# Optimization experiments

Measured on AMD Instinct MI355X. Metric: run time of the kernel, lower is better.

The kernel has to match this reference:

```python
import jax, jax.numpy as jnp
import numpy as np

BINS = jnp.array([1, 2, 3, 4, 8, 16, 32, 64], dtype=jnp.int32)
L = 10      # max span width
HID = 150   # Score hidden dim


def _mlp(x, W1, b1, W2, b2, W3, b3):
    # Score module: Linear -> ReLU -> Linear -> ReLU -> Linear (dropout = identity at eval)
    h = jax.nn.relu(x @ W1 + b1)
    h = jax.nn.relu(h @ W2 + b2)
    return h @ W3 + b3


def setup_inputs() -> dict:
    key = jax.random.key(0)
    ks = jax.random.split(key, 16)
    T, A, E, D, S = 8192, 1024, 512, 20, 32768
    GI = 2 * A + E + D  # 2580
    sc = lambda n: 1.0 / np.sqrt(n)
    return {
        "states": jax.random.normal(ks[0], (T, A), jnp.float32),
        "embeds": jax.random.normal(ks[1], (T, E), jnp.float32),
        "span_starts": jnp.sort(jax.random.randint(ks[2], (S,), 0, T - L)),
        "span_lengths": jax.random.randint(ks[3], (S,), 0, L),
        # attention Score params (attn_dim -> 150 -> 150 -> 1)
        "Wa1": jax.random.normal(ks[4], (A, HID), jnp.float32) * sc(A),
        "ba1": jnp.zeros((HID,), jnp.float32),
        "Wa2": jax.random.normal(ks[5], (HID, HID), jnp.float32) * sc(HID),
        "ba2": jnp.zeros((HID,), jnp.float32),
        "Wa3": jax.random.normal(ks[6], (HID, 1), jnp.float32) * sc(HID),
        "ba3": jnp.zeros((1,), jnp.float32),
        # Distance embedding table (len(bins)+1 = 9 buckets)
        "width_table": jax.random.normal(ks[7], (9, D), jnp.float32) * 0.1,
        # mention Score params (gi_dim -> 150 -> 150 -> 1)
        "Ws1": jax.random.normal(ks[8], (GI, HID), jnp.float32) * sc(GI),
        "bs1": jnp.zeros((HID,), jnp.float32),
        "Ws2": jax.random.normal(ks[9], (HID, HID), jnp.float32) * sc(HID),
        "bs2": jnp.zeros((HID,), jnp.float32),
        "Ws3": jax.random.normal(ks[10], (HID, 1), jnp.float32) * sc(HID),
        "bs3": jnp.zeros((1,), jnp.float32),
    }


def reference(states, embeds, span_starts, span_lengths,
              Wa1, ba1, Wa2, ba2, Wa3, ba3,
              width_table,
              Ws1, bs1, Ws2, bs2, Ws3, bs3):
    T = states.shape[0]
    # per-token attention logits: [T, 1]
    attns = _mlp(states, Wa1, ba1, Wa2, ba2, Wa3, ba3)

    pos = jnp.arange(L)
    idx = span_starts[:, None] + pos[None, :]                 # [S, L]
    mask = pos[None, :] <= span_lengths[:, None]              # valid positions
    idx = jnp.minimum(idx, T - 1)

    span_attn = jnp.where(mask, attns[idx, 0], -jnp.inf)      # [S, L]
    w = jax.nn.softmax(span_attn, axis=1)                     # per-span softmax
    pooled = jnp.einsum('sl,sle->se', w, embeds[idx])         # [S, E]

    ends = span_starts + span_lengths
    widths = span_lengths + 1
    bucket = jnp.searchsorted(BINS, widths.astype(jnp.int32), side='right')
    size_emb = width_table[bucket]                            # [S, D]

    g = jnp.concatenate([states[span_starts], states[ends], pooled, size_emb], axis=-1)
    scores = _mlp(g, Ws1, bs1, Ws2, bs2, Ws3, bs3)[:, 0]      # [S]
    return scores
```

## Files before the change

### kernel.cpp

```cpp
#include <hip/hip_runtime.h>
#include <math.h>

#define T_TOK 8192
#define A_DIM 1024
#define E_DIM 512
#define S_SPAN 32768
#define HID 150

typedef __attribute__((ext_vector_type(8))) short short8;
typedef __attribute__((ext_vector_type(4))) float f32x4;
typedef __attribute__((ext_vector_type(4))) unsigned int u32x4;
typedef __attribute__((ext_vector_type(4))) unsigned short u16x4;

__device__ __forceinline__ unsigned short f2bf(float f) {
    unsigned int u = __builtin_bit_cast(unsigned int, f);
    u += 0x7FFFu + ((u >> 16) & 1u);
    return (unsigned short)(u >> 16);
}
__device__ __forceinline__ float bf2f(unsigned int h16) {
    unsigned int u = h16 << 16;
    return __builtin_bit_cast(float, u);
}

#define NS4 (T_TOK * A_DIM / 4)
#define NE4 (T_TOK * E_DIM / 4)
#define NCAST ((NS4 + NE4) / 256)

struct WConv { const float* src; unsigned short* dst; int K0; int Kpad; int nblk; };
struct PrepTab {
    const float* s; const float* e; unsigned short* sd; unsigned short* ed;
    WConv g[6];
    const float* wt; const float* Ws1w; float* PW;
};

__global__ __launch_bounds__(256) void prep_kernel(PrepTab tab) {
    int b = blockIdx.x;
    if (b < NCAST) {
        int idx = b * 256 + threadIdx.x;
        const float* src; unsigned short* dst;
        if (idx < NS4) { src = tab.s; dst = tab.sd; }
        else { idx -= NS4; src = tab.e; dst = tab.ed; }
        f32x4 v = *(const f32x4*)(src + (size_t)idx * 4);
        u16x4 o;
        o.x = f2bf(v.x); o.y = f2bf(v.y); o.z = f2bf(v.z); o.w = f2bf(v.w);
        *(u16x4*)(dst + (size_t)idx * 4) = o;
        return;
    }
    b -= NCAST;
    #pragma unroll
    for (int gi = 0; gi < 6; ++gi) {
        if (b < tab.g[gi].nblk) {
            int idx = b * 256 + threadIdx.x;
            int Kpad = tab.g[gi].Kpad;
            if (idx < Kpad * 160) {
                int k = idx / 160, j = idx - k * 160;
                float v = (j < HID && k < tab.g[gi].K0)
                          ? tab.g[gi].src[(size_t)k * HID + j] : 0.f;
                tab.g[gi].dst[(size_t)j * Kpad + k] = f2bf(v);
            }
            return;
        }
        b -= tab.g[gi].nblk;
    }
    int j = threadIdx.x;
    if (j < HID) {
        float acc = 0.f;
        for (int k = 0; k < 20; ++k)
            acc = fmaf(tab.wt[b * 20 + k], tab.Ws1w[k * HID + j], acc);
        tab.PW[b * HID + j] = acc;
    }
}

struct GG {
    const unsigned short* A; int lda;
    const unsigned short* W; int K; int nrb;
    unsigned short* outh; int ldo;
    const float* bias; int relu;
    const float* dotv; const float* dotb; float* dotout;
};
struct GTab { GG g[4]; int ng; };

template <int TAG>
__global__ __launch_bounds__(256) void gemm_fused(GTab tab) {
    constexpr int LDW = 72;
    __shared__ unsigned short WtL[2][160 * LDW];

    int b = blockIdx.x;
    int gi = 0;
    while (gi < tab.ng - 1 && b >= tab.g[gi].nrb) { b -= tab.g[gi].nrb; ++gi; }
    const GG G = tab.g[gi];

    const int tid = threadIdx.x;
    const int wid = tid >> 6;
    const int lane = tid & 63;
    const int l15 = lane & 15;
    const int quad = lane >> 4;
    const int row0 = b * 64 + wid * 16 + l15;
    const int K = G.K;
    const int nch = K >> 6;
    const unsigned short* Arow = G.A + (size_t)row0 * G.lda;

    u32x4 stg[5];
    int sn[5], sk[5];
    #pragma unroll
    for (int i = 0; i < 5; ++i) { int u = tid + i * 256; sn[i] = u >> 3; sk[i] = (u & 7) * 8; }

    f32x4 acc[10];
    #pragma unroll
    for (int nt = 0; nt < 10; ++nt) acc[nt] = (f32x4){0.f, 0.f, 0.f, 0.f};

    #pragma unroll
    for (int i = 0; i < 5; ++i)
        stg[i] = *(const u32x4*)(G.W + (size_t)sn[i] * K + sk[i]);
    short8 avc0 = *(const short8*)(Arow + quad * 8);
    short8 avc1 = *(const short8*)(Arow + 32 + quad * 8);
    #pragma unroll
    for (int i = 0; i < 5; ++i)
        *(u32x4*)&WtL[0][sn[i] * LDW + sk[i]] = stg[i];
    __syncthreads();

    for (int c = 0; c < nch; ++c) {
        const int pb = c & 1;
        short8 avn0, avn1;
        const bool more = (c + 1 < nch);
        if (more) {
            const int kn = (c + 1) << 6;
            #pragma unroll
            for (int i = 0; i < 5; ++i)
                stg[i] = *(const u32x4*)(G.W + (size_t)sn[i] * K + kn + sk[i]);
            avn0 = *(const short8*)(Arow + kn + quad * 8);
            avn1 = *(const short8*)(Arow + kn + 32 + quad * 8);
        }
        #pragma unroll
        for (int nt = 0; nt < 10; ++nt) {
            short8 bv0 = *(const short8*)&WtL[pb][(nt * 16 + l15) * LDW + quad * 8];
            acc[nt] = __builtin_amdgcn_mfma_f32_16x16x32_bf16(avc0, bv0, acc[nt], 0, 0, 0);
            short8 bv1 = *(const short8*)&WtL[pb][(nt * 16 + l15) * LDW + 32 + quad * 8];
            acc[nt] = __builtin_amdgcn_mfma_f32_16x16x32_bf16(avc1, bv1, acc[nt], 0, 0, 0);
        }
        if (more) {
            #pragma unroll
            for (int i = 0; i < 5; ++i)
                *(u32x4*)&WtL[pb ^ 1][sn[i] * LDW + sk[i]] = stg[i];
            avc0 = avn0; avc1 = avn1;
        }
        __syncthreads();
    }

    const int rbase = b * 64 + wid * 16 + quad * 4;
    if (G.dotout) {
        float part[4] = {0.f, 0.f, 0.f, 0.f};
        #pragma unroll
        for (int nt = 0; nt < 10; ++nt) {
            int col = nt * 16 + l15;
            float bv_ = (col < HID) ? G.bias[col] : 0.f;
            float vv = (col < HID) ? G.dotv[col] : 0.f;
            #pragma unroll
            for (int r = 0; r < 4; ++r)
                part[r] += fmaxf(acc[nt][r] + bv_, 0.f) * vv;
        }
        #pragma unroll
        for (int r = 0; r < 4; ++r) {
            float p = part[r];
            #pragma unroll
            for (int off = 1; off < 16; off <<= 1) p += __shfl_xor(p, off);
            if (l15 == 0) G.dotout[rbase + r] = p + G.dotb[0];
        }
    } else {
        #pragma unroll
        for (int nt = 0; nt < 10; ++nt) {
            int col = nt * 16 + l15;
            float bv_ = (G.bias != nullptr && col < HID) ? G.bias[col] : 0.f;
            #pragma unroll
            for (int r = 0; r < 4; ++r) {
                int row = rbase + r;
                float v = acc[nt][r] + bv_;
                if (G.relu) v = fmaxf(v, 0.f);
                G.outh[(size_t)row * G.ldo + col] = f2bf(v);
            }
        }
    }
}

__global__ __launch_bounds__(256) void span_l1_kernel(const float* __restrict__ attns,
                                                      const int* __restrict__ starts,
                                                      const int* __restrict__ lens,
                                                      const unsigned short* __restrict__ Ps,
                                                      const unsigned short* __restrict__ Pe,
                                                      const unsigned short* __restrict__ Pm,
                                                      const float* __restrict__ PW,
                                                      const float* __restrict__ bs1,
                                                      unsigned short* __restrict__ SH1) {
    const int wid = threadIdx.x >> 6, lane = threadIdx.x & 63;
    const int s = blockIdx.x * 4 + wid;
    const int start = starts[s];
    const int len = lens[s];

    const int iv = min(start + lane, T_TOK - 1);
    float a = (lane <= len) ? attns[iv] : -INFINITY;
    float m = a;
    #pragma unroll
    for (int off = 32; off; off >>= 1) m = fmaxf(m, __shfl_xor(m, off));
    float e = (lane <= len) ? __expf(a - m) : 0.f;
    float ssum = e;
    #pragma unroll
    for (int off = 32; off; off >>= 1) ssum += __shfl_xor(ssum, off);
    float wv = e / ssum;

    float wl[10]; int il[10];
    #pragma unroll
    for (int l = 0; l < 10; ++l) { wl[l] = __shfl(wv, l); il[l] = __shfl(iv, l); }

    const int end = start + len;
    const int width = len + 1;
    const int bucket = (width >= 1) + (width >= 2) + (width >= 3) + (width >= 4) +
                       (width >= 8) + (width >= 16) + (width >= 32) + (width >= 64);

    const unsigned short* ps = Ps + (size_t)start * 160;
    const unsigned short* pe = Pe + (size_t)end * 160;
    const float* pw = PW + bucket * HID;

    for (int p = lane; p < 75; p += 64) {
        const int j = 2 * p;
        unsigned int u0 = *(const unsigned int*)(ps + j);
        unsigned int u1 = *(const unsigned int*)(pe + j);
        float a0 = bs1[j]     + bf2f(u0 & 0xffff) + bf2f(u1 & 0xffff) + pw[j];
        float a1 = bs1[j + 1] + bf2f(u0 >> 16)    + bf2f(u1 >> 16)    + pw[j + 1];
        #pragma unroll
        for (int l = 0; l < 10; ++l) {
            unsigned int um = *(const unsigned int*)(Pm + (size_t)il[l] * 160 + j);
            a0 = fmaf(wl[l], bf2f(um & 0xffff), a0);
            a1 = fmaf(wl[l], bf2f(um >> 16), a1);
        }
        unsigned int packed = (unsigned int)f2bf(fmaxf(a0, 0.f)) |
                              ((unsigned int)f2bf(fmaxf(a1, 0.f)) << 16);
        *(unsigned int*)(SH1 + (size_t)s * 192 + j) = packed;
    }
}

extern "C" void kernel_launch(void* const* d_in, const int* in_sizes, int n_in,
                              void* d_out, int out_size, void* d_ws, size_t ws_size,
                              hipStream_t stream) {
    const float* states = (const float*)d_in[0];
    const float* embeds = (const float*)d_in[1];
    const int* span_starts = (const int*)d_in[2];
    const int* span_lengths = (const int*)d_in[3];
    const float* Wa1 = (const float*)d_in[4];
    const float* ba1 = (const float*)d_in[5];
    const float* Wa2 = (const float*)d_in[6];
    const float* ba2 = (const float*)d_in[7];
    const float* Wa3 = (const float*)d_in[8];
    const float* ba3 = (const float*)d_in[9];
    const float* width_table = (const float*)d_in[10];
    const float* Ws1 = (const float*)d_in[11];
    const float* bs1 = (const float*)d_in[12];
    const float* Ws2 = (const float*)d_in[13];
    const float* bs2 = (const float*)d_in[14];
    const float* Ws3 = (const float*)d_in[15];
    const float* bs3 = (const float*)d_in[16];
    float* out = (float*)d_out;

    char* w = (char*)d_ws;
    unsigned short* WtA  = (unsigned short*)w;  w += 480 * 1024 * 2;
    unsigned short* WtE  = (unsigned short*)w;  w += 160 * 512 * 2;
    unsigned short* Wa2t = (unsigned short*)w;  w += 160 * 192 * 2;
    unsigned short* Ws2t = (unsigned short*)w;  w += 160 * 192 * 2;
    float* PW    = (float*)w;                   w += 5632;
    float* attns = (float*)w;                   w += 8192 * 4;
    unsigned short* Sbf = (unsigned short*)w;   w += (size_t)T_TOK * A_DIM * 2;
    unsigned short* Ebf = (unsigned short*)w;   w += (size_t)T_TOK * E_DIM * 2;
    unsigned short* Psh = (unsigned short*)w;   w += (size_t)T_TOK * 160 * 2;
    unsigned short* Peh = (unsigned short*)w;   w += (size_t)T_TOK * 160 * 2;
    unsigned short* Pmh = (unsigned short*)w;   w += (size_t)T_TOK * 160 * 2;
    unsigned short* H1A = (unsigned short*)w;   w += (size_t)T_TOK * 192 * 2;
    unsigned short* SH1 = (unsigned short*)w;   w += (size_t)S_SPAN * 192 * 2;

    PrepTab pt;
    pt.s = states; pt.e = embeds; pt.sd = Sbf; pt.ed = Ebf;
    pt.g[0] = { Wa1,              WtA,              1024, 1024, (160*1024 + 255)/256 };
    pt.g[1] = { Ws1,              WtA + 160*1024,   1024, 1024, (160*1024 + 255)/256 };
    pt.g[2] = { Ws1 + 1024*150,   WtA + 320*1024,   1024, 1024, (160*1024 + 255)/256 };
    pt.g[3] = { Ws1 + 2048*150,   WtE,               512,  512, (160*512  + 255)/256 };
    pt.g[4] = { Wa2,              Wa2t,              150,  192, (160*192  + 255)/256 };
    pt.g[5] = { Ws2,              Ws2t,              150,  192, (160*192  + 255)/256 };
    pt.wt = width_table; pt.Ws1w = Ws1 + 2560*150; pt.PW = PW;
    int wblk = 0; for (int i = 0; i < 6; ++i) wblk += pt.g[i].nblk;
    prep_kernel<<<NCAST + wblk + 9, 256, 0, stream>>>(pt);

    GG z = {};

    GTab t1; t1.ng = 4;
    t1.g[0] = z; t1.g[0].A = Sbf; t1.g[0].lda = 1024; t1.g[0].W = WtA;            t1.g[0].K = 1024;
    t1.g[0].nrb = 128; t1.g[0].outh = H1A; t1.g[0].ldo = 192; t1.g[0].bias = ba1; t1.g[0].relu = 1;
    t1.g[1] = z; t1.g[1].A = Sbf; t1.g[1].lda = 1024; t1.g[1].W = WtA + 160*1024; t1.g[1].K = 1024;
    t1.g[1].nrb = 128; t1.g[1].outh = Psh; t1.g[1].ldo = 160;
    t1.g[2] = z; t1.g[2].A = Sbf; t1.g[2].lda = 1024; t1.g[2].W = WtA + 320*1024; t1.g[2].K = 1024;
    t1.g[2].nrb = 128; t1.g[2].outh = Peh; t1.g[2].ldo = 160;
    t1.g[3] = z; t1.g[3].A = Ebf; t1.g[3].lda = 512;  t1.g[3].W = WtE;            t1.g[3].K = 512;
    t1.g[3].nrb = 128; t1.g[3].outh = Pmh; t1.g[3].ldo = 160;
    gemm_fused<1><<<512, 256, 0, stream>>>(t1);

    GTab t2; t2.ng = 1;
    t2.g[0] = z; t2.g[0].A = H1A; t2.g[0].lda = 192; t2.g[0].W = Wa2t; t2.g[0].K = 192;
    t2.g[0].nrb = 128; t2.g[0].bias = ba2; t2.g[0].dotv = Wa3; t2.g[0].dotb = ba3; t2.g[0].dotout = attns;
    gemm_fused<2><<<128, 256, 0, stream>>>(t2);

    span_l1_kernel<<<S_SPAN / 4, 256, 0, stream>>>(attns, span_starts, span_lengths,
                                                   Psh, Peh, Pmh, PW, bs1, SH1);

    GTab t3; t3.ng = 1;
    t3.g[0] = z; t3.g[0].A = SH1; t3.g[0].lda = 192; t3.g[0].W = Ws2t; t3.g[0].K = 192;
    t3.g[0].nrb = 512; t3.g[0].bias = bs2; t3.g[0].dotv = Ws3; t3.g[0].dotb = bs3; t3.g[0].dotout = out;
    gemm_fused<3><<<512, 256, 0, stream>>>(t3);
}
```

Before: 179.7 us.

## Fuse span pooling/layer-1 with layer-2 GEMM and score dot into one kernel

Merges the per-span softmax pooling and first-layer kernel with the second-layer MFMA GEMM and final dot-product. Each block builds a 64-span bf16 hidden tile directly in LDS, then multiplies it against a double-buffered Ws2 tile to produce scores. This removes the SH1 global round trip (32768x192 bf16 written and reread) and one launch. In exchange, each wave now handles 16 spans serially, and the grid is only 512 blocks with large LDS use, which may lower occupancy and latency hiding for the gather phase.

Result: slower. 190.5 us (+6.0%).

```diff
diff --git a/kernel.cpp b/kernel.cpp
--- a/kernel.cpp
+++ b/kernel.cpp
@@ -182,59 +182,139 @@
     }
 }
 
-__global__ __launch_bounds__(256) void span_l1_kernel(const float* __restrict__ attns,
-                                                      const int* __restrict__ starts,
-                                                      const int* __restrict__ lens,
-                                                      const unsigned short* __restrict__ Ps,
-                                                      const unsigned short* __restrict__ Pe,
-                                                      const unsigned short* __restrict__ Pm,
-                                                      const float* __restrict__ PW,
-                                                      const float* __restrict__ bs1,
-                                                      unsigned short* __restrict__ SH1) {
-    const int wid = threadIdx.x >> 6, lane = threadIdx.x & 63;
-    const int s = blockIdx.x * 4 + wid;
-    const int start = starts[s];
-    const int len = lens[s];
-
-    const int iv = min(start + lane, T_TOK - 1);
-    float a = (lane <= len) ? attns[iv] : -INFINITY;
-    float m = a;
-    #pragma unroll
-    for (int off = 32; off; off >>= 1) m = fmaxf(m, __shfl_xor(m, off));
-    float e = (lane <= len) ? __expf(a - m) : 0.f;
-    float ssum = e;
-    #pragma unroll
-    for (int off = 32; off; off >>= 1) ssum += __shfl_xor(ssum, off);
-    float wv = e / ssum;
-
-    float wl[10]; int il[10];
-    #pragma unroll
-    for (int l = 0; l < 10; ++l) { wl[l] = __shfl(wv, l); il[l] = __shfl(iv, l); }
-
-    const int end = start + len;
-    const int width = len + 1;
-    const int bucket = (width >= 1) + (width >= 2) + (width >= 3) + (width >= 4) +
-                       (width >= 8) + (width >= 16) + (width >= 32) + (width >= 64);
-
-    const unsigned short* ps = Ps + (size_t)start * 160;
-    const unsigned short* pe = Pe + (size_t)end * 160;
-    const float* pw = PW + bucket * HID;
-
-    for (int p = lane; p < 75; p += 64) {
-        const int j = 2 * p;
-        unsigned int u0 = *(const unsigned int*)(ps + j);
-        unsigned int u1 = *(const unsigned int*)(pe + j);
-        float a0 = bs1[j]     + bf2f(u0 & 0xffff) + bf2f(u1 & 0xffff) + pw[j];
-        float a1 = bs1[j + 1] + bf2f(u0 >> 16)    + bf2f(u1 >> 16)    + pw[j + 1];
-        #pragma unroll
-        for (int l = 0; l < 10; ++l) {
-            unsigned int um = *(const unsigned int*)(Pm + (size_t)il[l] * 160 + j);
-            a0 = fmaf(wl[l], bf2f(um & 0xffff), a0);
-            a1 = fmaf(wl[l], bf2f(um >> 16), a1);
-        }
-        unsigned int packed = (unsigned int)f2bf(fmaxf(a0, 0.f)) |
-                              ((unsigned int)f2bf(fmaxf(a1, 0.f)) << 16);
-        *(unsigned int*)(SH1 + (size_t)s * 192 + j) = packed;
+__global__ __launch_bounds__(256) void span_gemm_kernel(
+        const float* __restrict__ attns,
+        const int* __restrict__ starts, const int* __restrict__ lens,
+        const unsigned short* __restrict__ Ps, const unsigned short* __restrict__ Pe,
+        const unsigned short* __restrict__ Pm,
+        const float* __restrict__ PW, const float* __restrict__ bs1,
+        const unsigned short* __restrict__ W, const float* __restrict__ bs2,
+        const float* __restrict__ Ws3, const float* __restrict__ bs3,
+        float* __restrict__ out) {
+    constexpr int LDW = 72;
+    constexpr int LDA = 200;
+    __shared__ unsigned short WtL[2][160 * LDW];
+    __shared__ unsigned short Atile[64 * LDA];
+
+    const int tid = threadIdx.x;
+    const int wid = tid >> 6;
+    const int lane = tid & 63;
+    const int l15 = lane & 15;
+    const int quad = lane >> 4;
+    constexpr int K = 192;
+
+    u32x4 stg[5];
+    int sn[5], sk[5];
+    #pragma unroll
+    for (int i = 0; i < 5; ++i) { int u = tid + i * 256; sn[i] = u >> 3; sk[i] = (u & 7) * 8; }
+    #pragma unroll
+    for (int i = 0; i < 5; ++i)
+        stg[i] = *(const u32x4*)(W + (size_t)sn[i] * K + sk[i]);
+
+    for (int sp = 0; sp < 16; ++sp) {
+        const int sl = wid * 16 + sp;
+        const int s = blockIdx.x * 64 + sl;
+        const int start = starts[s];
+        const int len = lens[s];
+
+        const int iv = min(start + lane, T_TOK - 1);
+        float a = (lane <= len) ? attns[iv] : -INFINITY;
+        float m = a;
+        #pragma unroll
+        for (int off = 32; off; off >>= 1) m = fmaxf(m, __shfl_xor(m, off));
+        float e = (lane <= len) ? __expf(a - m) : 0.f;
+        float ssum = e;
+        #pragma unroll
+        for (int off = 32; off; off >>= 1) ssum += __shfl_xor(ssum, off);
+        float wv = e / ssum;
+
+        float wl[10]; int il[10];
+        #pragma unroll
+        for (int l = 0; l < 10; ++l) { wl[l] = __shfl(wv, l); il[l] = __shfl(iv, l); }
+
+        const int end = start + len;
+        const int width = len + 1;
+        const int bucket = (width >= 1) + (width >= 2) + (width >= 3) + (width >= 4) +
+                           (width >= 8) + (width >= 16) + (width >= 32) + (width >= 64);
+
+        const unsigned short* ps = Ps + (size_t)start * 160;
+        const unsigned short* pe = Pe + (size_t)end * 160;
+        const float* pw = PW + bucket * HID;
+
+        for (int p = lane; p < 96; p += 64) {
+            unsigned int packed = 0;
+            if (p < 75) {
+                const int j = 2 * p;
+                unsigned int u0 = *(const unsigned int*)(ps + j);
+                unsigned int u1 = *(const unsigned int*)(pe + j);
+                float a0 = bs1[j]     + bf2f(u0 & 0xffff) + bf2f(u1 & 0xffff) + pw[j];
+                float a1 = bs1[j + 1] + bf2f(u0 >> 16)    + bf2f(u1 >> 16)    + pw[j + 1];
+                #pragma unroll
+                for (int l = 0; l < 10; ++l) {
+                    unsigned int um = *(const unsigned int*)(Pm + (size_t)il[l] * 160 + j);
+                    a0 = fmaf(wl[l], bf2f(um & 0xffff), a0);
+                    a1 = fmaf(wl[l], bf2f(um >> 16), a1);
+                }
+                packed = (unsigned int)f2bf(fmaxf(a0, 0.f)) |
+                         ((unsigned int)f2bf(fmaxf(a1, 0.f)) << 16);
+            }
+            *(unsigned int*)&Atile[sl * LDA + 2 * p] = packed;
+        }
+    }
+
+    #pragma unroll
+    for (int i = 0; i < 5; ++i)
+        *(u32x4*)&WtL[0][sn[i] * LDW + sk[i]] = stg[i];
+    __syncthreads();
+
+    const int arow = wid * 16 + l15;
+    f32x4 acc[10];
+    #pragma unroll
+    for (int nt = 0; nt < 10; ++nt) acc[nt] = (f32x4){0.f, 0.f, 0.f, 0.f};
+
+    for (int c = 0; c < 3; ++c) {
+        const int pb = c & 1;
+        const bool more = (c + 1 < 3);
+        if (more) {
+            const int kn = (c + 1) << 6;
+            #pragma unroll
+            for (int i = 0; i < 5; ++i)
+                stg[i] = *(const u32x4*)(W + (size_t)sn[i] * K + kn + sk[i]);
+        }
+        short8 avc0 = *(const short8*)&Atile[arow * LDA + (c << 6) + quad * 8];
+        short8 avc1 = *(const short8*)&Atile[arow * LDA + (c << 6) + 32 + quad * 8];
+        #pragma unroll
+        for (int nt = 0; nt < 10; ++nt) {
+            short8 bv0 = *(const short8*)&WtL[pb][(nt * 16 + l15) * LDW + quad * 8];
+            acc[nt] = __builtin_amdgcn_mfma_f32_16x16x32_bf16(avc0, bv0, acc[nt], 0, 0, 0);
+            short8 bv1 = *(const short8*)&WtL[pb][(nt * 16 + l15) * LDW + 32 + quad * 8];
+            acc[nt] = __builtin_amdgcn_mfma_f32_16x16x32_bf16(avc1, bv1, acc[nt], 0, 0, 0);
+        }
+        if (more) {
+            #pragma unroll
+            for (int i = 0; i < 5; ++i)
+                *(u32x4*)&WtL[pb ^ 1][sn[i] * LDW + sk[i]] = stg[i];
+        }
+        __syncthreads();
+    }
+
+    float part[4] = {0.f, 0.f, 0.f, 0.f};
+    #pragma unroll
+    for (int nt = 0; nt < 10; ++nt) {
+        int col = nt * 16 + l15;
+        float bv_ = (col < HID) ? bs2[col] : 0.f;
+        float vv = (col < HID) ? Ws3[col] : 0.f;
+        #pragma unroll
+        for (int r = 0; r < 4; ++r)
+            part[r] += fmaxf(acc[nt][r] + bv_, 0.f) * vv;
+    }
+    const int rbase = blockIdx.x * 64 + wid * 16 + quad * 4;
+    #pragma unroll
+    for (int r = 0; r < 4; ++r) {
+        float p = part[r];
+        #pragma unroll
+        for (int off = 1; off < 16; off <<= 1) p += __shfl_xor(p, off);
+        if (l15 == 0) out[rbase + r] = p + bs3[0];
     }
 }
 
@@ -273,7 +353,6 @@
     unsigned short* Peh = (unsigned short*)w;   w += (size_t)T_TOK * 160 * 2;
     unsigned short* Pmh = (unsigned short*)w;   w += (size_t)T_TOK * 160 * 2;
     unsigned short* H1A = (unsigned short*)w;   w += (size_t)T_TOK * 192 * 2;
-    unsigned short* SH1 = (unsigned short*)w;   w += (size_t)S_SPAN * 192 * 2;
 
     PrepTab pt;
     pt.s = states; pt.e = embeds; pt.sd = Sbf; pt.ed = Ebf;
@@ -305,11 +384,7 @@
     t2.g[0].nrb = 128; t2.g[0].bias = ba2; t2.g[0].dotv = Wa3; t2.g[0].dotb = ba3; t2.g[0].dotout = attns;
     gemm_fused<2><<<128, 256, 0, stream>>>(t2);
 
-    span_l1_kernel<<<S_SPAN / 4, 256, 0, stream>>>(attns, span_starts, span_lengths,
-                                                   Psh, Peh, Pmh, PW, bs1, SH1);
-
-    GTab t3; t3.ng = 1;
-    t3.g[0] = z; t3.g[0].A = SH1; t3.g[0].lda = 192; t3.g[0].W = Ws2t; t3.g[0].K = 192;
-    t3.g[0].nrb = 512; t3.g[0].bias = bs2; t3.g[0].dotv = Ws3; t3.g[0].dotb = bs3; t3.g[0].dotout = out;
-    gemm_fused<3><<<512, 256, 0, stream>>>(t3);
-}
+    span_gemm_kernel<<<512, 256, 0, stream>>>(attns, span_starts, span_lengths,
+                                              Psh, Peh, Pmh, PW, bs1,
+                                              Ws2t, bs2, Ws3, bs3, out);
+}
```

## Retile GEMM warps into 2x2 grid of 32 rows by 80 columns

Applied to the files above, without the earlier changes.

Each warp previously computed 16 rows across all 160 output columns, so every warp read the full weight tile from LDS. Now warps form a 2x2 grid: each covers 32 rows and half the columns. Every B fragment loaded from LDS is reused for two MFMAs, which halves LDS weight reads per MFMA. In exchange each warp loads twice as many A rows from global memory, and the fused dot-product epilogue needs a shared-memory reduction across column halves plus an extra barrier.

New measurement: 181.3 us. No clear change (+0.9%).

```diff
diff --git a/kernel.cpp b/kernel.cpp
--- a/kernel.cpp
+++ b/kernel.cpp
@@ -84,6 +84,7 @@
 __global__ __launch_bounds__(256) void gemm_fused(GTab tab) {
     constexpr int LDW = 72;
     __shared__ unsigned short WtL[2][160 * LDW];
+    __shared__ float dsum[64];
 
     int b = blockIdx.x;
     int gi = 0;
@@ -95,25 +96,32 @@
     const int lane = tid & 63;
     const int l15 = lane & 15;
     const int quad = lane >> 4;
-    const int row0 = b * 64 + wid * 16 + l15;
+    const int g = wid >> 1;
+    const int h = wid & 1;
+    const int row0 = b * 64 + g * 32 + l15;
     const int K = G.K;
     const int nch = K >> 6;
-    const unsigned short* Arow = G.A + (size_t)row0 * G.lda;
+    const unsigned short* Arow0 = G.A + (size_t)row0 * G.lda;
+    const unsigned short* Arow1 = G.A + (size_t)(row0 + 16) * G.lda;
 
     u32x4 stg[5];
     int sn[5], sk[5];
     #pragma unroll
     for (int i = 0; i < 5; ++i) { int u = tid + i * 256; sn[i] = u >> 3; sk[i] = (u & 7) * 8; }
 
-    f32x4 acc[10];
-    #pragma unroll
-    for (int nt = 0; nt < 10; ++nt) acc[nt] = (f32x4){0.f, 0.f, 0.f, 0.f};
+    f32x4 acc[2][5];
+    #pragma unroll
+    for (int mt = 0; mt < 2; ++mt)
+        #pragma unroll
+        for (int nt = 0; nt < 5; ++nt) acc[mt][nt] = (f32x4){0.f, 0.f, 0.f, 0.f};
 
     #pragma unroll
     for (int i = 0; i < 5; ++i)
         stg[i] = *(const u32x4*)(G.W + (size_t)sn[i] * K + sk[i]);
-    short8 avc0 = *(const short8*)(Arow + quad * 8);
-    short8 avc1 = *(const short8*)(Arow + 32 + quad * 8);
+    short8 a00 = *(const short8*)(Arow0 + quad * 8);
+    short8 a01 = *(const short8*)(Arow0 + 32 + quad * 8);
+    short8 a10 = *(const short8*)(Arow1 + quad * 8);
+    short8 a11 = *(const short8*)(Arow1 + 32 + quad * 8);
     #pragma unroll
     for (int i = 0; i < 5; ++i)
         *(u32x4*)&WtL[0][sn[i] * LDW + sk[i]] = stg[i];
@@ -121,63 +129,93 @@
 
     for (int c = 0; c < nch; ++c) {
         const int pb = c & 1;
-        short8 avn0, avn1;
+        short8 n00, n01, n10, n11;
         const bool more = (c + 1 < nch);
         if (more) {
             const int kn = (c + 1) << 6;
             #pragma unroll
             for (int i = 0; i < 5; ++i)
                 stg[i] = *(const u32x4*)(G.W + (size_t)sn[i] * K + kn + sk[i]);
-            avn0 = *(const short8*)(Arow + kn + quad * 8);
-            avn1 = *(const short8*)(Arow + kn + 32 + quad * 8);
-        }
-        #pragma unroll
-        for (int nt = 0; nt < 10; ++nt) {
-            short8 bv0 = *(const short8*)&WtL[pb][(nt * 16 + l15) * LDW + quad * 8];
-            acc[nt] = __builtin_amdgcn_mfma_f32_16x16x32_bf16(avc0, bv0, acc[nt], 0, 0, 0);
-            short8 bv1 = *(const short8*)&WtL[pb][(nt * 16 + l15) * LDW + 32 + quad * 8];
-            acc[nt] = __builtin_amdgcn_mfma_f32_16x16x32_bf16(avc1, bv1, acc[nt], 0, 0, 0);
+            n00 = *(const short8*)(Arow0 + kn + quad * 8);
+            n01 = *(const short8*)(Arow0 + kn + 32 + quad * 8);
+            n10 = *(const short8*)(Arow1 + kn + quad * 8);
+            n11 = *(const short8*)(Arow1 + kn + 32 + quad * 8);
+        }
+        #pragma unroll
+        for (int nt = 0; nt < 5; ++nt) {
+            const int wrow = (h * 80 + nt * 16 + l15) * LDW;
+            short8 bv0 = *(const short8*)&WtL[pb][wrow + quad * 8];
+            acc[0][nt] = __builtin_amdgcn_mfma_f32_16x16x32_bf16(a00, bv0, acc[0][nt], 0, 0, 0);
+            acc[1][nt] = __builtin_amdgcn_mfma_f32_16x16x32_bf16(a10, bv0, acc[1][nt], 0, 0, 0);
+            short8 bv1 = *(const short8*)&WtL[pb][wrow + 32 + quad * 8];
+            acc[0][nt] = __builtin_amdgcn_mfma_f32_16x16x32_bf16(a01, bv1, acc[0][nt], 0, 0, 0);
+            acc[1][nt] = __builtin_amdgcn_mfma_f32_16x16x32_bf16(a11, bv1, acc[1][nt], 0, 0, 0);
         }
         if (more) {
             #pragma unroll
             for (int i = 0; i < 5; ++i)
                 *(u32x4*)&WtL[pb ^ 1][sn[i] * LDW + sk[i]] = stg[i];
-            avc0 = avn0; avc1 = avn1;
+            a00 = n00; a01 = n01; a10 = n10; a11 = n11;
         }
         __syncthreads();
     }
 
-    const int rbase = b * 64 + wid * 16 + quad * 4;
     if (G.dotout) {
-        float part[4] = {0.f, 0.f, 0.f, 0.f};
-        #pragma unroll
-        for (int nt = 0; nt < 10; ++nt) {
-            int col = nt * 16 + l15;
+        float part[2][4];
+        #pragma unroll
+        for (int mt = 0; mt < 2; ++mt)
+            #pragma unroll
+            for (int r = 0; r < 4; ++r) part[mt][r] = 0.f;
+        #pragma unroll
+        for (int nt = 0; nt < 5; ++nt) {
+            int col = h * 80 + nt * 16 + l15;
             float bv_ = (col < HID) ? G.bias[col] : 0.f;
             float vv = (col < HID) ? G.dotv[col] : 0.f;
             #pragma unroll
-            for (int r = 0; r < 4; ++r)
-                part[r] += fmaxf(acc[nt][r] + bv_, 0.f) * vv;
-        }
-        #pragma unroll
-        for (int r = 0; r < 4; ++r) {
-            float p = part[r];
-            #pragma unroll
-            for (int off = 1; off < 16; off <<= 1) p += __shfl_xor(p, off);
-            if (l15 == 0) G.dotout[rbase + r] = p + G.dotb[0];
+            for (int mt = 0; mt < 2; ++mt)
+                #pragma unroll
+                for (int r = 0; r < 4; ++r)
+                    part[mt][r] += fmaxf(acc[mt][nt][r] + bv_, 0.f) * vv;
+        }
+        #pragma unroll
+        for (int mt = 0; mt < 2; ++mt)
+            #pragma unroll
+            for (int r = 0; r < 4; ++r) {
+                #pragma unroll
+                for (int off = 1; off < 16; off <<= 1)
+                    part[mt][r] += __shfl_xor(part[mt][r], off);
+            }
+        if (h == 0 && l15 == 0) {
+            #pragma unroll
+            for (int mt = 0; mt < 2; ++mt)
+                #pragma unroll
+                for (int r = 0; r < 4; ++r)
+                    dsum[g * 32 + mt * 16 + quad * 4 + r] = part[mt][r];
+        }
+        __syncthreads();
+        if (h == 1 && l15 == 0) {
+            #pragma unroll
+            for (int mt = 0; mt < 2; ++mt)
+                #pragma unroll
+                for (int r = 0; r < 4; ++r) {
+                    int lr = g * 32 + mt * 16 + quad * 4 + r;
+                    G.dotout[b * 64 + lr] = dsum[lr] + part[mt][r] + G.dotb[0];
+                }
         }
     } else {
         #pragma unroll
-        for (int nt = 0; nt < 10; ++nt) {
-            int col = nt * 16 + l15;
+        for (int nt = 0; nt < 5; ++nt) {
+            int col = h * 80 + nt * 16 + l15;
             float bv_ = (G.bias != nullptr && col < HID) ? G.bias[col] : 0.f;
             #pragma unroll
-            for (int r = 0; r < 4; ++r) {
-                int row = rbase + r;
-                float v = acc[nt][r] + bv_;
-                if (G.relu) v = fmaxf(v, 0.f);
-                G.outh[(size_t)row * G.ldo + col] = f2bf(v);
-            }
+            for (int mt = 0; mt < 2; ++mt)
+                #pragma unroll
+                for (int r = 0; r < 4; ++r) {
+                    int row = b * 64 + g * 32 + mt * 16 + quad * 4 + r;
+                    float v = acc[mt][nt][r] + bv_;
+                    if (G.relu) v = fmaxf(v, 0.f);
+                    G.outh[(size_t)row * G.ldo + col] = f2bf(v);
+                }
         }
     }
 }
```
